# Kernel optimization log

Measured on AMD Instinct MI355X. Metric: run time of the kernel, lower is better.

Reference implementation:

```python
import jax, jax.numpy as jnp
import numpy as np

B, S, H, NH = 4, 2048, 2048, 16
HD = H // NH
EPS = 1e-5


def setup_inputs() -> dict:
    key = jax.random.key(0)
    ks = jax.random.split(key, 5)
    return {
        "x": jax.random.normal(ks[0], (B, S, H), dtype=jnp.float32),
        "ln_w": jnp.ones((H,), dtype=jnp.float32),
        "ln_b": jnp.zeros((H,), dtype=jnp.float32),
        "c_attn_w": jax.random.normal(ks[1], (H, 3 * H), dtype=jnp.float32) * 0.02,
        "c_attn_b": jax.random.normal(ks[2], (3 * H,), dtype=jnp.float32) * 0.02,
        "c_proj_w": jax.random.normal(ks[3], (H, H), dtype=jnp.float32) * 0.02,
        "c_proj_b": jax.random.normal(ks[4], (H,), dtype=jnp.float32) * 0.02,
    }


def reference(x, ln_w, ln_b, c_attn_w, c_attn_b, c_proj_w, c_proj_b):
    residual = x
    # fused layer norm
    mu = jnp.mean(x, axis=-1, keepdims=True)
    var = jnp.mean(jnp.square(x - mu), axis=-1, keepdims=True)
    xn = (x - mu) * jax.lax.rsqrt(var + EPS) * ln_w + ln_b
    qkv = jnp.einsum("bsh,hk->bsk", xn, c_attn_w) + c_attn_b
    q, k, v = jnp.split(qkv, 3, axis=-1)
    def heads(t):
        return t.reshape(B, S, NH, HD).transpose(0, 2, 1, 3)
    q, k, v = heads(q), heads(k), heads(v)
    # causal flash attention (reference math)
    scale = 1.0 / np.sqrt(HD)
    scores = jnp.einsum("bnqd,bnkd->bnqk", q, k) * scale
    causal = jnp.tril(jnp.ones((S, S), dtype=bool))
    scores = jnp.where(causal, scores, jnp.finfo(scores.dtype).min)
    attn = jax.nn.softmax(scores, axis=-1)
    o = jnp.einsum("bnqk,bnkd->bnqd", attn, v)
    # merge heads: [B,NH,S,HD] -> [B,S,H]
    o = o.transpose(0, 2, 1, 3).reshape(B, S, H)
    # output projection + residual (fused_ffn, add_gelu=False, dropout=0)
    return jnp.einsum("bsh,hk->bsk", o, c_proj_w) + c_proj_b + residual
```

## Files before the change

kernel.cpp:

```cpp
#include <hip/hip_runtime.h>
#include <stdint.h>
#include <math.h>

#define B_  4
#define S_  2048
#define H_  2048
#define NH_ 16
#define HD_ 128
#define M_  (B_*S_)
#define N3_ (3*H_)
#define NQT_ (S_/64)
#define NT_ (H_/64)

typedef __attribute__((ext_vector_type(8))) short short8;
typedef __attribute__((ext_vector_type(4))) float floatx4;
typedef unsigned int u32;

__device__ __forceinline__ unsigned short f2bf(float f) {
  unsigned u = __float_as_uint(f);
  u += 0x7FFF + ((u >> 16) & 1);
  return (unsigned short)(u >> 16);
}

__device__ __forceinline__ void gl2lds16(const void* g, void* l) {
  __builtin_amdgcn_global_load_lds(
      (const __attribute__((address_space(1))) u32*)g,
      (__attribute__((address_space(3))) u32*)l, 16, 0, 0);
}

__global__ __launch_bounds__(256) void ln_kernel(
    const float* __restrict__ x, const float* __restrict__ w,
    const float* __restrict__ b, unsigned short* __restrict__ xn) {
  int row = blockIdx.x;
  int t = threadIdx.x;
  const float* xr = x + (size_t)row * H_;
  float4 v0 = *(const float4*)(xr + t * 4);
  float4 v1 = *(const float4*)(xr + 1024 + t * 4);
  float s  = v0.x + v0.y + v0.z + v0.w + v1.x + v1.y + v1.z + v1.w;
  float sq = v0.x*v0.x + v0.y*v0.y + v0.z*v0.z + v0.w*v0.w
           + v1.x*v1.x + v1.y*v1.y + v1.z*v1.z + v1.w*v1.w;
  #pragma unroll
  for (int m = 32; m; m >>= 1) { s += __shfl_xor(s, m); sq += __shfl_xor(sq, m); }
  __shared__ float red[8];
  int wv = t >> 6;
  if ((t & 63) == 0) { red[wv * 2] = s; red[wv * 2 + 1] = sq; }
  __syncthreads();
  s  = red[0] + red[2] + red[4] + red[6];
  sq = red[1] + red[3] + red[5] + red[7];
  float mu  = s * (1.0f / H_);
  float var = sq * (1.0f / H_) - mu * mu;
  float rs  = rsqrtf(var + 1e-5f);

  float4 w0 = *(const float4*)(w + t * 4);
  float4 b0 = *(const float4*)(b + t * 4);
  float4 w1 = *(const float4*)(w + 1024 + t * 4);
  float4 b1 = *(const float4*)(b + 1024 + t * 4);
  ushort4 o0, o1;
  o0.x = f2bf((v0.x - mu) * rs * w0.x + b0.x);
  o0.y = f2bf((v0.y - mu) * rs * w0.y + b0.y);
  o0.z = f2bf((v0.z - mu) * rs * w0.z + b0.z);
  o0.w = f2bf((v0.w - mu) * rs * w0.w + b0.w);
  o1.x = f2bf((v1.x - mu) * rs * w1.x + b1.x);
  o1.y = f2bf((v1.y - mu) * rs * w1.y + b1.y);
  o1.z = f2bf((v1.z - mu) * rs * w1.z + b1.z);
  o1.w = f2bf((v1.w - mu) * rs * w1.w + b1.w);
  unsigned short* orow = xn + (size_t)row * H_;
  *(ushort4*)(orow + t * 4) = o0;
  *(ushort4*)(orow + 1024 + t * 4) = o1;
}

__global__ __launch_bounds__(256) void transpose_f2b(
    const float* __restrict__ in, unsigned short* __restrict__ out,
    int R, int C) {
  __shared__ float tile[32][33];
  int tx = threadIdx.x & 31, ty = threadIdx.x >> 5;
  int c0 = blockIdx.x * 32, r0 = blockIdx.y * 32;
  #pragma unroll
  for (int i = 0; i < 32; i += 8)
    tile[ty + i][tx] = in[(size_t)(r0 + ty + i) * C + c0 + tx];
  __syncthreads();
  #pragma unroll
  for (int i = 0; i < 32; i += 8)
    out[(size_t)(c0 + ty + i) * R + r0 + tx] = f2bf(tile[tx][ty + i]);
}

__device__ __forceinline__ void gemm256_acc(
    const unsigned short* __restrict__ A, const unsigned short* __restrict__ Bt,
    int m0, int n0, unsigned short (*sh)[16384], floatx4 (&acc)[8][4]) {
  const int t = threadIdx.x;
  const int lane = t & 63, wv = t >> 6;
  const int l15 = lane & 15, quad = lane >> 4;
  const int wm = wv >> 2, wn = wv & 3;
  const int x7 = l15 & 7;

  const int aRB = (wm * 128 + l15) * 64;
  const int bRB = (wn * 64 + l15) * 64;
  const int kx0 = ((0 + quad) ^ x7) * 8;
  const int kx1 = ((4 + quad) ^ x7) * 8;

  const int r = t >> 3, cc = t & 7;
  const int scol = (cc ^ (r & 7)) * 8;
  const unsigned short* aSrc = A + (size_t)(m0 + r) * H_ + scol;
  const int btr = (r >> 5) * 64 + (r & 31);
  const unsigned short* bSrc = Bt + (size_t)(n0 + btr) * H_ + scol;
  const int aDst = t * 8;
  const int bDst = (r >> 5) * 4096 + (r & 31) * 64 + cc * 8;

  auto stageA = [&](int kt, int reg, int buf) {
    const unsigned short* s = aSrc + (size_t)(reg * 64) * H_ + kt * 64;
    unsigned short* d = sh[buf * 2] + aDst + reg * 4096;
    gl2lds16(s, d);
    gl2lds16(s + (size_t)128 * H_, d + 8192);
  };
  auto stageB = [&](int kt, int reg, int buf) {
    const unsigned short* s = bSrc + (size_t)(reg * 32) * H_ + kt * 64;
    unsigned short* d = sh[buf * 2 + 1] + bDst + reg * 2048;
    gl2lds16(s, d);
    gl2lds16(s + (size_t)128 * H_, d + 8192);
  };

  #pragma unroll
  for (int i = 0; i < 8; i++)
    #pragma unroll
    for (int j = 0; j < 4; j++) acc[i][j] = (floatx4){0.f, 0.f, 0.f, 0.f};

  stageA(0, 0, 0); stageB(0, 0, 0); stageA(0, 1, 0); stageB(0, 1, 0);
  stageA(1, 0, 1); stageB(1, 0, 1); stageA(1, 1, 1);
  asm volatile("s_waitcnt vmcnt(6)" ::: "memory");
  __builtin_amdgcn_s_barrier();

  short8 aR[4][2], b01[2][2], b23[2][2];

  for (int n = 0; n < NT_; ++n) {
    const int buf = n & 1;
    const unsigned short* Ab = sh[buf * 2];
    const unsigned short* Bb = sh[buf * 2 + 1];

    #pragma unroll
    for (int i = 0; i < 4; ++i) {
      aR[i][0] = *(const short8*)(Ab + aRB + i * 1024 + kx0);
      aR[i][1] = *(const short8*)(Ab + aRB + i * 1024 + kx1);
    }
    #pragma unroll
    for (int j = 0; j < 2; ++j) {
      b01[j][0] = *(const short8*)(Bb + bRB + j * 1024 + kx0);
      b01[j][1] = *(const short8*)(Bb + bRB + j * 1024 + kx1);
    }
    if (n + 1 < NT_) stageB(n + 1, 1, buf ^ 1);
    asm volatile("s_waitcnt lgkmcnt(8)" ::: "memory");
    __builtin_amdgcn_s_barrier();
    asm volatile("s_waitcnt lgkmcnt(0)" ::: "memory");
    __builtin_amdgcn_sched_barrier(0);
    __builtin_amdgcn_s_setprio(1);
    #pragma unroll
    for (int i = 0; i < 4; ++i)
      #pragma unroll
      for (int j = 0; j < 2; ++j) {
        acc[i][j] = __builtin_amdgcn_mfma_f32_16x16x32_bf16(aR[i][0], b01[j][0], acc[i][j], 0, 0, 0);
        acc[i][j] = __builtin_amdgcn_mfma_f32_16x16x32_bf16(aR[i][1], b01[j][1], acc[i][j], 0, 0, 0);
      }
    __builtin_amdgcn_s_setprio(0);
    __builtin_amdgcn_s_barrier();

    #pragma unroll
    for (int j = 0; j < 2; ++j) {
      b23[j][0] = *(const short8*)(Bb + bRB + (j + 2) * 1024 + kx0);
      b23[j][1] = *(const short8*)(Bb + bRB + (j + 2) * 1024 + kx1);
    }
    if (n + 2 < NT_) stageA(n + 2, 0, buf);
    __builtin_amdgcn_s_barrier();
    asm volatile("s_waitcnt lgkmcnt(0)" ::: "memory");
    __builtin_amdgcn_sched_barrier(0);
    __builtin_amdgcn_s_setprio(1);
    #pragma unroll
    for (int i = 0; i < 4; ++i)
      #pragma unroll
      for (int j = 0; j < 2; ++j) {
        acc[i][j + 2] = __builtin_amdgcn_mfma_f32_16x16x32_bf16(aR[i][0], b23[j][0], acc[i][j + 2], 0, 0, 0);
        acc[i][j + 2] = __builtin_amdgcn_mfma_f32_16x16x32_bf16(aR[i][1], b23[j][1], acc[i][j + 2], 0, 0, 0);
      }
    __builtin_amdgcn_s_setprio(0);
    __builtin_amdgcn_s_barrier();

    #pragma unroll
    for (int i = 0; i < 4; ++i) {
      aR[i][0] = *(const short8*)(Ab + aRB + (i + 4) * 1024 + kx0);
      aR[i][1] = *(const short8*)(Ab + aRB + (i + 4) * 1024 + kx1);
    }
    if (n + 2 < NT_) stageB(n + 2, 0, buf);
    __builtin_amdgcn_s_barrier();
    asm volatile("s_waitcnt lgkmcnt(0)" ::: "memory");
    __builtin_amdgcn_sched_barrier(0);
    __builtin_amdgcn_s_setprio(1);
    #pragma unroll
    for (int i = 0; i < 4; ++i)
      #pragma unroll
      for (int j = 0; j < 2; ++j) {
        acc[i + 4][j] = __builtin_amdgcn_mfma_f32_16x16x32_bf16(aR[i][0], b01[j][0], acc[i + 4][j], 0, 0, 0);
        acc[i + 4][j] = __builtin_amdgcn_mfma_f32_16x16x32_bf16(aR[i][1], b01[j][1], acc[i + 4][j], 0, 0, 0);
      }
    __builtin_amdgcn_s_setprio(0);
    __builtin_amdgcn_s_barrier();

    if (n + 2 < NT_) stageA(n + 2, 1, buf);
    __builtin_amdgcn_s_barrier();
    __builtin_amdgcn_s_setprio(1);
    #pragma unroll
    for (int i = 0; i < 4; ++i)
      #pragma unroll
      for (int j = 0; j < 2; ++j) {
        acc[i + 4][j + 2] = __builtin_amdgcn_mfma_f32_16x16x32_bf16(aR[i][0], b23[j][0], acc[i + 4][j + 2], 0, 0, 0);
        acc[i + 4][j + 2] = __builtin_amdgcn_mfma_f32_16x16x32_bf16(aR[i][1], b23[j][1], acc[i + 4][j + 2], 0, 0, 0);
      }
    __builtin_amdgcn_s_setprio(0);
    if (n + 2 < NT_) asm volatile("s_waitcnt vmcnt(6)" ::: "memory");
    else             asm volatile("s_waitcnt vmcnt(0)" ::: "memory");
    __builtin_amdgcn_s_barrier();
  }
}

__device__ __forceinline__ void xcd_map(int& m0, int& n0) {
  int bid = blockIdx.y * gridDim.x + blockIdx.x;
  int xcd = bid & 7, loc = bid >> 3;
  m0 = ((xcd << 2) | (loc & 3)) * 256;
  n0 = (loc >> 2) * 256;
}

__global__ __launch_bounds__(512, 2) void qkv_gemm(
    const unsigned short* __restrict__ A, const unsigned short* __restrict__ Bt,
    const float* __restrict__ bias,
    unsigned short* __restrict__ qw, unsigned short* __restrict__ kw,
    unsigned short* __restrict__ vtw) {
  __shared__ unsigned short sh[4][16384];
  int m0, n0;
  xcd_map(m0, n0);

  floatx4 acc[8][4];
  gemm256_acc(A, Bt, m0, n0, sh, acc);

  int t = threadIdx.x, lane = t & 63, wv = t >> 6;
  int l15 = lane & 15, quad = lane >> 4;
  int wm = wv >> 2, wn = wv & 3;
  int sec = n0 >> 11;
  #pragma unroll
  for (int j = 0; j < 4; ++j) {
    int nn = n0 + wn * 64 + j * 16 + l15;
    int h = (nn >> 7) & 15;
    int d = nn & 127;
    float bval = bias[nn];
    #pragma unroll
    for (int i = 0; i < 8; ++i) {
      int m = m0 + wm * 128 + i * 16 + quad * 4;
      int bb = m >> 11, s = m & 2047;
      int bh = bb * NH_ + h;
      if (sec == 2) {
        ushort4 pv;
        pv.x = f2bf(acc[i][j][0] + bval); pv.y = f2bf(acc[i][j][1] + bval);
        pv.z = f2bf(acc[i][j][2] + bval); pv.w = f2bf(acc[i][j][3] + bval);
        *(ushort4*)(vtw + ((size_t)bh * HD_ + d) * S_ + s) = pv;
      } else {
        unsigned short* dst = (sec == 0 ? qw : kw) + ((size_t)bh * S_ + s) * HD_ + d;
        #pragma unroll
        for (int reg = 0; reg < 4; reg++)
          dst[(size_t)reg * HD_] = f2bf(acc[i][j][reg] + bval);
      }
    }
  }
}

__global__ __launch_bounds__(512, 2) void proj_gemm(
    const unsigned short* __restrict__ A, const unsigned short* __restrict__ Bt,
    const float* __restrict__ bias, const float* __restrict__ resid,
    float* __restrict__ out) {
  __shared__ unsigned short sh[4][16384];
  int m0, n0;
  xcd_map(m0, n0);

  floatx4 acc[8][4];
  gemm256_acc(A, Bt, m0, n0, sh, acc);

  int t = threadIdx.x, lane = t & 63, wv = t >> 6;
  int l15 = lane & 15, quad = lane >> 4;
  int wm = wv >> 2, wn = wv & 3;
  #pragma unroll
  for (int j = 0; j < 4; ++j) {
    int nn = n0 + wn * 64 + j * 16 + l15;
    float bval = bias[nn];
    #pragma unroll
    for (int i = 0; i < 8; ++i) {
      int m = m0 + wm * 128 + i * 16 + quad * 4;
      #pragma unroll
      for (int reg = 0; reg < 4; ++reg)
        out[(size_t)(m + reg) * H_ + nn] =
            acc[i][j][reg] + bval + resid[(size_t)(m + reg) * H_ + nn];
    }
  }
}

__global__ __launch_bounds__(256) void attn_kernel(
    const unsigned short* __restrict__ qw, const unsigned short* __restrict__ kw,
    const unsigned short* __restrict__ vtw, unsigned short* __restrict__ ow) {
  __shared__ unsigned short Klds[64 * 136];
  __shared__ unsigned short Vtl[128 * 72];
  __shared__ unsigned short Pl[4][16 * 72];
  int pr = blockIdx.x, bh = blockIdx.y;
  int t = threadIdx.x, lane = t & 63, wv = t >> 6;
  int l15 = lane & 15, quad = lane >> 4;
  int h = bh & 15, bb = bh >> 4;

  const float scale = 0.08838834764831845f;
  int krr = t >> 4, kcc = (t & 15) * 8;
  int vdd = t >> 3, vss = (t & 7) * 8;
  unsigned short* plw = &Pl[wv][0];
  const unsigned short* kgb = kw + ((size_t)bh * S_ + krr) * HD_ + kcc;
  const unsigned short* vgb = vtw + ((size_t)bh * HD_ + vdd) * S_ + vss;

  short8 kreg[4], vreg[4];
  auto load_stage = [&](int kb) {
    #pragma unroll
    for (int c = 0; c < 4; c++) {
      kreg[c] = *(const short8*)(kgb + (size_t)(kb + c * 16) * HD_);
      vreg[c] = *(const short8*)(vgb + (size_t)(c * 32) * S_ + kb);
    }
  };

  #pragma unroll 1
  for (int half = 0; half < 2; half++) {
    int qt = half ? (NQT_ - 1 - pr) : pr;
    int qr = qt * 64 + wv * 16;
    int q = qr + l15;

    short8 qf[4];
    {
      const unsigned short* qbase = qw + ((size_t)bh * S_ + q) * HD_ + quad * 8;
      #pragma unroll
      for (int ks = 0; ks < 4; ks++)
        qf[ks] = *(const short8*)(qbase + ks * 32);
    }

    float m_i = -INFINITY, l_i = 0.f;
    floatx4 o[8];
    #pragma unroll
    for (int ht = 0; ht < 8; ht++) o[ht] = (floatx4){0.f, 0.f, 0.f, 0.f};

    load_stage(0);
    #pragma unroll 1
    for (int kt = 0; kt <= qt; kt++) {
      int kb = kt * 64;
      __syncthreads();
      #pragma unroll
      for (int c = 0; c < 4; c++) {
        *(short8*)(Klds + (c * 16 + krr) * 136 + kcc) = kreg[c];
        *(short8*)(Vtl + (c * 32 + vdd) * 72 + vss) = vreg[c];
      }
      __syncthreads();
      if (kt < qt) load_stage(kb + 64);

      floatx4 sv[4];
      __builtin_amdgcn_s_setprio(1);
      #pragma unroll
      for (int jm = 0; jm < 4; jm++) {
        sv[jm] = (floatx4){0.f, 0.f, 0.f, 0.f};
        #pragma unroll
        for (int ks = 0; ks < 4; ks++) {
          short8 kf = *(const short8*)(Klds + (jm * 16 + l15) * 136 + ks * 32 + quad * 8);
          sv[jm] = __builtin_amdgcn_mfma_f32_16x16x32_bf16(kf, qf[ks], sv[jm], 0, 0, 0);
        }
      }
      __builtin_amdgcn_s_setprio(0);

      float p[4][4];
      float pmax = -INFINITY;
      #pragma unroll
      for (int jm = 0; jm < 4; jm++)
        #pragma unroll
        for (int reg = 0; reg < 4; reg++) {
          float v = sv[jm][reg] * scale;
          int key = kb + jm * 16 + quad * 4 + reg;
          if (key > q) v = -1e30f;
          p[jm][reg] = v;
          pmax = fmaxf(pmax, v);
        }
      pmax = fmaxf(pmax, __shfl_xor(pmax, 16));
      pmax = fmaxf(pmax, __shfl_xor(pmax, 32));
      if (!__all(pmax - m_i <= 8.f)) {
        float mnew = fmaxf(m_i, pmax);
        float alpha = __expf(m_i - mnew);
        l_i *= alpha;
        #pragma unroll
        for (int ht = 0; ht < 8; ht++) o[ht] *= alpha;
        m_i = mnew;
      }
      float sum = 0.f;
      #pragma unroll
      for (int jm = 0; jm < 4; jm++)
        #pragma unroll
        for (int reg = 0; reg < 4; reg++) { p[jm][reg] = __expf(p[jm][reg] - m_i); sum += p[jm][reg]; }
      sum += __shfl_xor(sum, 16);
      sum += __shfl_xor(sum, 32);
      l_i += sum;

      #pragma unroll
      for (int jm = 0; jm < 4; jm++) {
        ushort4 pk;
        pk.x = f2bf(p[jm][0]); pk.y = f2bf(p[jm][1]);
        pk.z = f2bf(p[jm][2]); pk.w = f2bf(p[jm][3]);
        *(ushort4*)(plw + l15 * 72 + jm * 16 + quad * 4) = pk;
      }

      __builtin_amdgcn_s_setprio(1);
      #pragma unroll
      for (int ks2 = 0; ks2 < 2; ks2++) {
        short8 pf = *(const short8*)(plw + l15 * 72 + ks2 * 32 + quad * 8);
        #pragma unroll
        for (int ht = 0; ht < 8; ht++) {
          short8 vf = *(const short8*)(Vtl + (ht * 16 + l15) * 72 + ks2 * 32 + quad * 8);
          o[ht] = __builtin_amdgcn_mfma_f32_16x16x32_bf16(vf, pf, o[ht], 0, 0, 0);
        }
      }
      __builtin_amdgcn_s_setprio(0);
    }

    float inv = 1.0f / l_i;
    size_t base = ((size_t)(bb * S_ + q)) * H_ + h * HD_ + quad * 4;
    #pragma unroll
    for (int ht = 0; ht < 8; ht++) {
      ushort4 ov;
      ov.x = f2bf(o[ht][0] * inv); ov.y = f2bf(o[ht][1] * inv);
      ov.z = f2bf(o[ht][2] * inv); ov.w = f2bf(o[ht][3] * inv);
      *(ushort4*)(ow + base + ht * 16) = ov;
    }
  }
}

extern "C" void kernel_launch(void* const* d_in, const int* in_sizes, int n_in,
                              void* d_out, int out_size, void* d_ws, size_t ws_size,
                              hipStream_t stream) {
  (void)in_sizes; (void)n_in; (void)out_size; (void)ws_size;
  const float* x      = (const float*)d_in[0];
  const float* ln_w   = (const float*)d_in[1];
  const float* ln_b   = (const float*)d_in[2];
  const float* attn_w = (const float*)d_in[3];
  const float* attn_b = (const float*)d_in[4];
  const float* proj_w = (const float*)d_in[5];
  const float* proj_b = (const float*)d_in[6];
  float* out = (float*)d_out;

  char* ws = (char*)d_ws;
  size_t off = 0;
  auto alloc = [&](size_t bytes) {
    char* p = ws + off;
    off += (bytes + 255) & ~(size_t)255;
    return p;
  };
  unsigned short* xn     = (unsigned short*)alloc((size_t)M_ * H_ * 2);
  unsigned short* wqkvt  = (unsigned short*)alloc((size_t)N3_ * H_ * 2);
  unsigned short* wprojt = (unsigned short*)alloc((size_t)H_ * H_ * 2);
  unsigned short* qws    = (unsigned short*)alloc((size_t)M_ * H_ * 2);
  unsigned short* kws    = (unsigned short*)alloc((size_t)M_ * H_ * 2);
  unsigned short* vtws   = (unsigned short*)alloc((size_t)M_ * H_ * 2);
  unsigned short* attn_out = xn;

  ln_kernel<<<M_, 256, 0, stream>>>(x, ln_w, ln_b, xn);
  transpose_f2b<<<dim3(N3_ / 32, H_ / 32), 256, 0, stream>>>(attn_w, wqkvt, H_, N3_);
  transpose_f2b<<<dim3(H_ / 32, H_ / 32), 256, 0, stream>>>(proj_w, wprojt, H_, H_);
  qkv_gemm<<<dim3(N3_ / 256, M_ / 256), 512, 0, stream>>>(xn, wqkvt, attn_b, qws, kws, vtws);
  attn_kernel<<<dim3(NQT_ / 2, B_ * NH_), 256, 0, stream>>>(qws, kws, vtws, attn_out);
  proj_gemm<<<dim3(H_ / 256, M_ / 256), 512, 0, stream>>>(attn_out, wprojt, proj_b, x, out);
}
```

Baseline: 625.2 us.

## Restructure GEMM main loop to one barrier per k-tile with register prefetch

Rewrites the GEMM inner loop so each k-tile issues all global-to-LDS copies for tile n+2 at once and uses a single barrier per iteration instead of about eight. A and B fragments are split into even/odd register sets and the next tile's fragments are read from LDS during the last MFMA block, overlapping LDS reads with compute. It needs more VGPRs for the extra fragment buffers, which could hurt occupancy at 2 blocks per CU. The vmcnt(0) wait before the barrier may also expose global load latency that the finer-grained staging used to hide.

```diff
diff --git a/kernel.cpp b/kernel.cpp
--- a/kernel.cpp
+++ b/kernel.cpp
@@ -106,17 +106,49 @@
   const int aDst = t * 8;
   const int bDst = (r >> 5) * 4096 + (r & 31) * 64 + cc * 8;
 
-  auto stageA = [&](int kt, int reg, int buf) {
-    const unsigned short* s = aSrc + (size_t)(reg * 64) * H_ + kt * 64;
-    unsigned short* d = sh[buf * 2] + aDst + reg * 4096;
-    gl2lds16(s, d);
-    gl2lds16(s + (size_t)128 * H_, d + 8192);
-  };
-  auto stageB = [&](int kt, int reg, int buf) {
-    const unsigned short* s = bSrc + (size_t)(reg * 32) * H_ + kt * 64;
-    unsigned short* d = sh[buf * 2 + 1] + bDst + reg * 2048;
-    gl2lds16(s, d);
-    gl2lds16(s + (size_t)128 * H_, d + 8192);
+  auto stageAll = [&](int kt, int buf) {
+    const unsigned short* sa = aSrc + kt * 64;
+    const unsigned short* sb = bSrc + kt * 64;
+    unsigned short* da = sh[buf * 2] + aDst;
+    unsigned short* db = sh[buf * 2 + 1] + bDst;
+    gl2lds16(sa, da);
+    gl2lds16(sa + (size_t)128 * H_, da + 8192);
+    gl2lds16(sa + (size_t)64 * H_, da + 4096);
+    gl2lds16(sa + (size_t)192 * H_, da + 12288);
+    gl2lds16(sb, db);
+    gl2lds16(sb + (size_t)128 * H_, db + 8192);
+    gl2lds16(sb + (size_t)32 * H_, db + 2048);
+    gl2lds16(sb + (size_t)160 * H_, db + 10240);
+  };
+
+  short8 aE[4][2], aO[4][2], b01[2][2], b23[2][2];
+  auto readAE = [&](const unsigned short* Ab) {
+    #pragma unroll
+    for (int i = 0; i < 4; ++i) {
+      aE[i][0] = *(const short8*)(Ab + aRB + i * 1024 + kx0);
+      aE[i][1] = *(const short8*)(Ab + aRB + i * 1024 + kx1);
+    }
+  };
+  auto readAO = [&](const unsigned short* Ab) {
+    #pragma unroll
+    for (int i = 0; i < 4; ++i) {
+      aO[i][0] = *(const short8*)(Ab + aRB + (i + 4) * 1024 + kx0);
+      aO[i][1] = *(const short8*)(Ab + aRB + (i + 4) * 1024 + kx1);
+    }
+  };
+  auto readB01 = [&](const unsigned short* Bb) {
+    #pragma unroll
+    for (int j = 0; j < 2; ++j) {
+      b01[j][0] = *(const short8*)(Bb + bRB + j * 1024 + kx0);
+      b01[j][1] = *(const short8*)(Bb + bRB + j * 1024 + kx1);
+    }
+  };
+  auto readB23 = [&](const unsigned short* Bb) {
+    #pragma unroll
+    for (int j = 0; j < 2; ++j) {
+      b23[j][0] = *(const short8*)(Bb + bRB + (j + 2) * 1024 + kx0);
+      b23[j][1] = *(const short8*)(Bb + bRB + (j + 2) * 1024 + kx1);
+    }
   };
 
   #pragma unroll
@@ -124,31 +156,43 @@
     #pragma unroll
     for (int j = 0; j < 4; j++) acc[i][j] = (floatx4){0.f, 0.f, 0.f, 0.f};
 
-  stageA(0, 0, 0); stageB(0, 0, 0); stageA(0, 1, 0); stageB(0, 1, 0);
-  stageA(1, 0, 1); stageB(1, 0, 1); stageA(1, 1, 1);
-  asm volatile("s_waitcnt vmcnt(6)" ::: "memory");
+  stageAll(0, 0);
+  stageAll(1, 1);
+  asm volatile("s_waitcnt vmcnt(8)" ::: "memory");
   __builtin_amdgcn_s_barrier();
-
-  short8 aR[4][2], b01[2][2], b23[2][2];
+  readAE(sh[0]); readB01(sh[1]);
 
   for (int n = 0; n < NT_; ++n) {
     const int buf = n & 1;
     const unsigned short* Ab = sh[buf * 2];
     const unsigned short* Bb = sh[buf * 2 + 1];
 
-    #pragma unroll
-    for (int i = 0; i < 4; ++i) {
-      aR[i][0] = *(const short8*)(Ab + aRB + i * 1024 + kx0);
-      aR[i][1] = *(const short8*)(Ab + aRB + i * 1024 + kx1);
-    }
-    #pragma unroll
-    for (int j = 0; j < 2; ++j) {
-      b01[j][0] = *(const short8*)(Bb + bRB + j * 1024 + kx0);
-      b01[j][1] = *(const short8*)(Bb + bRB + j * 1024 + kx1);
-    }
-    if (n + 1 < NT_) stageB(n + 1, 1, buf ^ 1);
+    readB23(Bb);
+    asm volatile("s_waitcnt lgkmcnt(4)" ::: "memory");
+    __builtin_amdgcn_sched_barrier(0);
+    __builtin_amdgcn_s_setprio(1);
+    #pragma unroll
+    for (int i = 0; i < 4; ++i)
+      #pragma unroll
+      for (int j = 0; j < 2; ++j) {
+        acc[i][j] = __builtin_amdgcn_mfma_f32_16x16x32_bf16(aE[i][0], b01[j][0], acc[i][j], 0, 0, 0);
+        acc[i][j] = __builtin_amdgcn_mfma_f32_16x16x32_bf16(aE[i][1], b01[j][1], acc[i][j], 0, 0, 0);
+      }
+    __builtin_amdgcn_s_setprio(0);
+
+    readAO(Ab);
     asm volatile("s_waitcnt lgkmcnt(8)" ::: "memory");
-    __builtin_amdgcn_s_barrier();
+    __builtin_amdgcn_sched_barrier(0);
+    __builtin_amdgcn_s_setprio(1);
+    #pragma unroll
+    for (int i = 0; i < 4; ++i)
+      #pragma unroll
+      for (int j = 0; j < 2; ++j) {
+        acc[i][j + 2] = __builtin_amdgcn_mfma_f32_16x16x32_bf16(aE[i][0], b23[j][0], acc[i][j + 2], 0, 0, 0);
+        acc[i][j + 2] = __builtin_amdgcn_mfma_f32_16x16x32_bf16(aE[i][1], b23[j][1], acc[i][j + 2], 0, 0, 0);
+      }
+    __builtin_amdgcn_s_setprio(0);
+
     asm volatile("s_waitcnt lgkmcnt(0)" ::: "memory");
     __builtin_amdgcn_sched_barrier(0);
     __builtin_amdgcn_s_setprio(1);
@@ -156,66 +200,25 @@
     for (int i = 0; i < 4; ++i)
       #pragma unroll
       for (int j = 0; j < 2; ++j) {
-        acc[i][j] = __builtin_amdgcn_mfma_f32_16x16x32_bf16(aR[i][0], b01[j][0], acc[i][j], 0, 0, 0);
-        acc[i][j] = __builtin_amdgcn_mfma_f32_16x16x32_bf16(aR[i][1], b01[j][1], acc[i][j], 0, 0, 0);
+        acc[i + 4][j] = __builtin_amdgcn_mfma_f32_16x16x32_bf16(aO[i][0], b01[j][0], acc[i + 4][j], 0, 0, 0);
+        acc[i + 4][j] = __builtin_amdgcn_mfma_f32_16x16x32_bf16(aO[i][1], b01[j][1], acc[i + 4][j], 0, 0, 0);
       }
     __builtin_amdgcn_s_setprio(0);
+
+    asm volatile("s_waitcnt vmcnt(0)" ::: "memory");
     __builtin_amdgcn_s_barrier();
-
-    #pragma unroll
-    for (int j = 0; j < 2; ++j) {
-      b23[j][0] = *(const short8*)(Bb + bRB + (j + 2) * 1024 + kx0);
-      b23[j][1] = *(const short8*)(Bb + bRB + (j + 2) * 1024 + kx1);
-    }
-    if (n + 2 < NT_) stageA(n + 2, 0, buf);
-    __builtin_amdgcn_s_barrier();
-    asm volatile("s_waitcnt lgkmcnt(0)" ::: "memory");
-    __builtin_amdgcn_sched_barrier(0);
+    if (n + 1 < NT_) { readAE(sh[(buf ^ 1) * 2]); readB01(sh[(buf ^ 1) * 2 + 1]); }
+    if (n + 2 < NT_) stageAll(n + 2, buf);
+
     __builtin_amdgcn_s_setprio(1);
     #pragma unroll
     for (int i = 0; i < 4; ++i)
       #pragma unroll
       for (int j = 0; j < 2; ++j) {
-        acc[i][j + 2] = __builtin_amdgcn_mfma_f32_16x16x32_bf16(aR[i][0], b23[j][0], acc[i][j + 2], 0, 0, 0);
-        acc[i][j + 2] = __builtin_amdgcn_mfma_f32_16x16x32_bf16(aR[i][1], b23[j][1], acc[i][j + 2], 0, 0, 0);
+        acc[i + 4][j + 2] = __builtin_amdgcn_mfma_f32_16x16x32_bf16(aO[i][0], b23[j][0], acc[i + 4][j + 2], 0, 0, 0);
+        acc[i + 4][j + 2] = __builtin_amdgcn_mfma_f32_16x16x32_bf16(aO[i][1], b23[j][1], acc[i + 4][j + 2], 0, 0, 0);
       }
     __builtin_amdgcn_s_setprio(0);
-    __builtin_amdgcn_s_barrier();
-
-    #pragma unroll
-    for (int i = 0; i < 4; ++i) {
-      aR[i][0] = *(const short8*)(Ab + aRB + (i + 4) * 1024 + kx0);
-      aR[i][1] = *(const short8*)(Ab + aRB + (i + 4) * 1024 + kx1);
-    }
-    if (n + 2 < NT_) stageB(n + 2, 0, buf);
-    __builtin_amdgcn_s_barrier();
-    asm volatile("s_waitcnt lgkmcnt(0)" ::: "memory");
-    __builtin_amdgcn_sched_barrier(0);
-    __builtin_amdgcn_s_setprio(1);
-    #pragma unroll
-    for (int i = 0; i < 4; ++i)
-      #pragma unroll
-      for (int j = 0; j < 2; ++j) {
-        acc[i + 4][j] = __builtin_amdgcn_mfma_f32_16x16x32_bf16(aR[i][0], b01[j][0], acc[i + 4][j], 0, 0, 0);
-        acc[i + 4][j] = __builtin_amdgcn_mfma_f32_16x16x32_bf16(aR[i][1], b01[j][1], acc[i + 4][j], 0, 0, 0);
-      }
-    __builtin_amdgcn_s_setprio(0);
-    __builtin_amdgcn_s_barrier();
-
-    if (n + 2 < NT_) stageA(n + 2, 1, buf);
-    __builtin_amdgcn_s_barrier();
-    __builtin_amdgcn_s_setprio(1);
-    #pragma unroll
-    for (int i = 0; i < 4; ++i)
-      #pragma unroll
-      for (int j = 0; j < 2; ++j) {
-        acc[i + 4][j + 2] = __builtin_amdgcn_mfma_f32_16x16x32_bf16(aR[i][0], b23[j][0], acc[i + 4][j + 2], 0, 0, 0);
-        acc[i + 4][j + 2] = __builtin_amdgcn_mfma_f32_16x16x32_bf16(aR[i][1], b23[j][1], acc[i + 4][j + 2], 0, 0, 0);
-      }
-    __builtin_amdgcn_s_setprio(0);
-    if (n + 2 < NT_) asm volatile("s_waitcnt vmcnt(6)" ::: "memory");
-    else             asm volatile("s_waitcnt vmcnt(0)" ::: "memory");
-    __builtin_amdgcn_s_barrier();
   }
 }
 
```

Result: faster. 610.1 us (-2.4%).
